# Kernel tuning notes

Hardware: AMD Instinct MI355X
Metric: run time of the kernel (lower is better)

Reference implementation:

```python
import jax, jax.numpy as jnp
import numpy as np

N_Q = 50000
B, T = 256, 500
DK = 128      # q_embed_dim == memory_key_state_dim == final_fc_dim
DV = 256      # qa_embed_dim == memory_value_state_dim
M = 50        # memory_size

def setup_inputs() -> dict:
    key = jax.random.key(0)
    ks = jax.random.split(key, 12)
    q_data = jax.random.randint(ks[0], (B, T), 0, N_Q + 1)
    qa_data = jax.random.randint(ks[1], (B, T), 0, 2 * N_Q + 1)
    # target in {-1, 0, 1}; -1 = padding (masked out)
    u = jax.random.uniform(ks[2], (B * T, 1))
    target = jnp.floor(u * 3.0) - 1.0
    # embedding tables with padding_idx=0 zeroed
    q_tab = (jax.random.normal(ks[3], (N_Q + 1, DK)) * (2.0 / DK) ** 0.5).at[0].set(0.0)
    qa_tab = (jax.random.normal(ks[4], (2 * N_Q + 1, DV)) * (2.0 / DV) ** 0.5).at[0].set(0.0)
    Mk = jax.random.normal(ks[5], (M, DK)) * (2.0 / DK) ** 0.5
    Mv0 = jax.random.normal(ks[6], (M, DV)) * (2.0 / DV) ** 0.5
    We = jax.random.normal(ks[7], (DV, DV)) * (1.0 / DV) ** 0.5
    be = jnp.zeros((DV,))
    Wa = jax.random.normal(ks[8], (DV, DV)) * (1.0 / DV) ** 0.5
    ba = jnp.zeros((DV,))
    Wr = jax.random.normal(ks[9], (DK, DV + DK)) * (2.0 / (DV + DK)) ** 0.5
    br = jnp.zeros((DK,))
    Wp = jax.random.normal(ks[10], (1, DK)) * (2.0 / DK) ** 0.5
    bp = jnp.zeros((1,))
    return dict(q_data=q_data, qa_data=qa_data, target=target, q_tab=q_tab,
                qa_tab=qa_tab, Mk=Mk, Mv0=Mv0, We=We, be=be, Wa=Wa, ba=ba,
                Wr=Wr, br=br, Wp=Wp, bp=bp)


def reference(q_data, qa_data, target, q_tab, qa_tab, Mk, Mv0, We, be, Wa, ba, Wr, br, Wp, bp):
    b, t = q_data.shape
    q_e = q_tab[q_data]            # (B,T,DK)
    qa_e = qa_tab[qa_data]         # (B,T,DV)
    wr_mask = (q_data >= 1).astype(q_e.dtype)  # write gate per step
    Mv_init = jnp.broadcast_to(Mv0[None], (b, M, DV))

    def step(Mv, xs):
        q, qa, m = xs              # q:(B,DK) qa:(B,DV) m:(B,)
        w = jax.nn.softmax(q @ Mk.T, axis=-1)          # (B,M) correlation weight
        read = jnp.einsum('bm,bmd->bd', w, Mv)         # (B,DV)
        e = jax.nn.sigmoid(qa @ We.T + be)             # erase (B,DV)
        a = jnp.tanh(qa @ Wa.T + ba)                   # add   (B,DV)
        new = Mv * (1.0 - w[:, :, None] * e[:, None, :]) + w[:, :, None] * a[:, None, :]
        Mv = jnp.where(m[:, None, None] > 0, new, Mv)  # only write for non-pad steps
        return Mv, read

    _, reads = jax.lax.scan(step, Mv_init,
                            (q_e.transpose(1, 0, 2), qa_e.transpose(1, 0, 2), wr_mask.T))
    reads = reads.transpose(1, 0, 2)                    # (B,T,DV)
    feat = jnp.concatenate([reads, q_e], axis=2).reshape(b * t, DV + DK)
    h = jnp.tanh(feat @ Wr.T + br)                      # (B*T,DK)
    pred = h @ Wp.T + bp                                # (B*T,1) logits
    mask = target >= 0
    # stable BCE-with-logits per element
    per = jnp.maximum(pred, 0.0) - pred * target + jnp.log1p(jnp.exp(-jnp.abs(pred)))
    n_valid = jnp.maximum(jnp.sum(mask.astype(pred.dtype)), 1.0)
    loss = jnp.sum(jnp.where(mask, per, 0.0)) / n_valid
    probs = jax.nn.sigmoid(pred)
    return loss, probs
```

## Files before the change

### kernel.cpp

```cpp
#include <hip/hip_runtime.h>
#include <hip/hip_bf16.h>
#include <stdint.h>


#define BATCH 256
#define TLEN  500
#define DKQ   128
#define DVV   256
#define MSZ   50
#define NROWS 128000
#define GSZ   10

__device__ __forceinline__ float bfs(uint16_t u){
  union { uint32_t u; float f; } v; v.u = ((uint32_t)u) << 16; return v.f;
}
__device__ __forceinline__ uint16_t f2b(float x){
  union { __hip_bfloat16 h; uint16_t u; } c; c.h = __float2bfloat16(x); return c.u;
}

typedef __attribute__((ext_vector_type(8))) short bf16x8;
typedef __attribute__((ext_vector_type(4))) float f32x4;

__device__ __forceinline__ void gl_lds16(const void* g, void* l){
  __builtin_amdgcn_global_load_lds(
      (const __attribute__((address_space(1))) void*)g,
      (__attribute__((address_space(3))) void*)l, 16, 0, 0);
}

__global__ __launch_bounds__(128, 1) void k_w(
    const int* __restrict__ q_data, const float* __restrict__ q_tab,
    const float* __restrict__ Mk, float* __restrict__ w_ws)
{
  __shared__ float mk[MSZ*DKQ];
  __shared__ float wt[128*52];
  const int tid = threadIdx.x;
  for (int li = tid; li < 1600; li += 128)
    ((float4*)mk)[li] = ((const float4*)Mk)[li];
  __syncthreads();

  const int row = blockIdx.x*128 + tid;
  const int qi = q_data[row];
  const float4* qrow = (const float4*)(q_tab + (size_t)qi*DKQ);

  float acc[MSZ];
  #pragma unroll
  for (int m=0;m<MSZ;m++) acc[m] = 0.f;

  #pragma unroll 1
  for (int c8=0; c8<8; c8++){
    float4 q0 = qrow[c8*4+0], q1 = qrow[c8*4+1], q2 = qrow[c8*4+2], q3 = qrow[c8*4+3];
    #pragma unroll
    for (int m=0;m<MSZ;m++){
      const float4* mr = (const float4*)&mk[m*DKQ + c8*16];
      float4 a = mr[0], b = mr[1], cc = mr[2], d = mr[3];
      float s = acc[m];
      s = fmaf(q0.x,a.x,s);  s = fmaf(q0.y,a.y,s);  s = fmaf(q0.z,a.z,s);  s = fmaf(q0.w,a.w,s);
      s = fmaf(q1.x,b.x,s);  s = fmaf(q1.y,b.y,s);  s = fmaf(q1.z,b.z,s);  s = fmaf(q1.w,b.w,s);
      s = fmaf(q2.x,cc.x,s); s = fmaf(q2.y,cc.y,s); s = fmaf(q2.z,cc.z,s); s = fmaf(q2.w,cc.w,s);
      s = fmaf(q3.x,d.x,s);  s = fmaf(q3.y,d.y,s);  s = fmaf(q3.z,d.z,s);  s = fmaf(q3.w,d.w,s);
      acc[m] = s;
    }
  }
  float mx = acc[0];
  #pragma unroll
  for (int m=1;m<MSZ;m++) mx = fmaxf(mx, acc[m]);
  float s = 0.f;
  #pragma unroll
  for (int m=0;m<MSZ;m++){ acc[m] = __expf(acc[m]-mx); s += acc[m]; }
  float inv = 1.0f / s;
  #pragma unroll
  for (int m=0;m<MSZ;m++) wt[tid*52+m] = acc[m]*inv;
  wt[tid*52+50] = 0.f; wt[tid*52+51] = 0.f;
  __syncthreads();
  float4* dst = (float4*)(w_ws + (size_t)blockIdx.x*128*52);
  const float4* src = (const float4*)wt;
  for (int li = tid; li < 1664; li += 128) dst[li] = src[li];
}

__global__ __launch_bounds__(256) void k_cvt(
    const float* __restrict__ qa_tab, const float* __restrict__ We,
    const float* __restrict__ Wa, uint16_t* __restrict__ qa_bf,
    uint16_t* __restrict__ wcomb)
{
  const size_t n_qa4 = 6400064;
  const size_t n_w4  = 32768;
  size_t stride = (size_t)gridDim.x*blockDim.x;
  for (size_t i = (size_t)blockIdx.x*256 + threadIdx.x; i < n_qa4 + n_w4; i += stride){
    float4 v;
    if (i < n_qa4){
      v = ((const float4*)qa_tab)[i];
      ushort4 o; o.x=f2b(v.x); o.y=f2b(v.y); o.z=f2b(v.z); o.w=f2b(v.w);
      ((ushort4*)qa_bf)[i] = o;
    } else {
      size_t j = i - n_qa4;
      size_t f = j*4;
      int col = (int)(f >> 8), k = (int)(f & 255);
      const float* srcp = (col < 256) ? (We + (size_t)col*256 + k)
                                      : (Wa + (size_t)(col-256)*256 + k);
      v = *(const float4*)srcp;
      ushort4 o; o.x=f2b(v.x); o.y=f2b(v.y); o.z=f2b(v.z); o.w=f2b(v.w);
      ((ushort4*)wcomb)[j] = o;
    }
  }
}

__global__ __launch_bounds__(256) void k_cvt2(
    const float* __restrict__ q_tab, const float* __restrict__ Wr,
    uint16_t* __restrict__ q_bf, uint16_t* __restrict__ wr_bf)
{
  const size_t n_q4  = 1600032;
  const size_t n_wr4 = 12288;
  size_t stride = (size_t)gridDim.x*blockDim.x;
  for (size_t i = (size_t)blockIdx.x*256 + threadIdx.x; i < n_q4 + n_wr4; i += stride){
    if (i < n_q4){
      float4 v = ((const float4*)q_tab)[i];
      ushort4 o; o.x=f2b(v.x); o.y=f2b(v.y); o.z=f2b(v.z); o.w=f2b(v.w);
      ((ushort4*)q_bf)[i] = o;
    } else {
      size_t j = i - n_q4;
      float4 v = ((const float4*)Wr)[j];
      ushort4 o; o.x=f2b(v.x); o.y=f2b(v.y); o.z=f2b(v.z); o.w=f2b(v.w);
      ((ushort4*)wr_bf)[j] = o;
    }
  }
}

__global__ __launch_bounds__(256, 2) void k_ea(
    const int* __restrict__ qa_data, const uint16_t* __restrict__ qa_bf,
    const uint16_t* __restrict__ wcomb, const float* __restrict__ be,
    const float* __restrict__ ba, __hip_bfloat16* __restrict__ ea_ws)
{
  __shared__ uint16_t Ab[128*32];
  __shared__ uint16_t Bb[128*32];
  const int tid = threadIdx.x;
  const int lane = tid & 63, wid = tid >> 6;
  const int braw = blockIdx.x;
  const int nb = (braw >> 3) & 3;
  const int mb = (braw & 7) | ((braw >> 5) << 3);
  const int rb = mb*128, cb = nb*128;

  const char* qac = (const char*)qa_bf;
  size_t aoff0, aoff1;
  {
    int r0 = wid*32 + (lane>>2);
    aoff0 = (size_t)qa_data[rb + r0]*512      + (size_t)(lane&3)*16;
    aoff1 = (size_t)qa_data[rb + r0 + 16]*512 + (size_t)(lane&3)*16;
  }
  const char* wcb = (const char*)wcomb;
  size_t boff0 = (size_t)(cb + wid*32 + (lane>>2))*512 + (size_t)(lane&3)*16;
  size_t boff1 = boff0 + 16*512;

  const int wr = (wid>>1)*64, wc = (wid&1)*64;
  float bias[4];
  #pragma unroll
  for (int tj=0;tj<4;tj++){
    int colg = cb + wc + tj*16 + (lane&15);
    bias[tj] = (nb<2) ? be[colg] : ba[colg-256];
  }

  f32x4 acc[4][4];
  #pragma unroll
  for (int i=0;i<4;i++){
    #pragma unroll
    for (int j=0;j<4;j++) acc[i][j] = (f32x4)(0.f);
  }

  #pragma unroll 1
  for (int kc=0; kc<8; kc++){
    __syncthreads();
    gl_lds16(qac + aoff0 + (size_t)kc*64, &Ab[(wid*2+0)*512]);
    gl_lds16(qac + aoff1 + (size_t)kc*64, &Ab[(wid*2+1)*512]);
    gl_lds16(wcb + boff0 + (size_t)kc*64, &Bb[(wid*2+0)*512]);
    gl_lds16(wcb + boff1 + (size_t)kc*64, &Bb[(wid*2+1)*512]);
    __syncthreads();
    bf16x8 af[4], bfr[4];
    #pragma unroll
    for (int ti=0;ti<4;ti++)
      af[ti] = *(const bf16x8*)&Ab[(wr + ti*16 + (lane&15))*32 + (lane>>4)*8];
    #pragma unroll
    for (int tj=0;tj<4;tj++)
      bfr[tj] = *(const bf16x8*)&Bb[(wc + tj*16 + (lane&15))*32 + (lane>>4)*8];
    #pragma unroll
    for (int ti=0;ti<4;ti++){
      #pragma unroll
      for (int tj=0;tj<4;tj++)
        acc[ti][tj] = __builtin_amdgcn_mfma_f32_16x16x32_bf16(af[ti], bfr[tj], acc[ti][tj], 0, 0, 0);
    }
  }
  const int rq = (lane>>4)*4, cl = lane&15;
  #pragma unroll
  for (int ti=0;ti<4;ti++){
    #pragma unroll
    for (int r=0;r<4;r++){
      int row = rb + wr + ti*16 + rq + r;
      __hip_bfloat16* orow = ea_ws + (size_t)row*512 + cb + wc;
      #pragma unroll
      for (int tj=0;tj<4;tj++){
        float x = acc[ti][tj][r] + bias[tj];
        float v = (nb<2) ? (1.f/(1.f+__expf(-x)))
                         : (1.f - 2.f/(__expf(2.f*x)+1.f));
        orow[tj*16 + cl] = __float2bfloat16(v);
      }
    }
  }
}

__global__ __launch_bounds__(256, 1) void k_scan(
    const int* __restrict__ q_data, const float* __restrict__ w_ws,
    const uint16_t* __restrict__ ea_ws, const float* __restrict__ Mv0,
    __hip_bfloat16* __restrict__ reads_ws)
{
  __shared__ __align__(16) float wlds[2][GSZ*52];
  const int tid  = threadIdx.x;
  const int d    = tid;
  const int b    = blockIdx.x;
  const int base = b * TLEN;

  float Mv[52];
  #pragma unroll
  for (int m=0;m<MSZ;m++) Mv[m] = Mv0[(size_t)m*256 + d];
  Mv[50] = 0.f; Mv[51] = 0.f;

  typedef const __attribute__((address_space(4))) int cint;
  cint* qbase = (cint*)q_data + base;

  const char* wsrc = (const char*)(w_ws + (size_t)base*52);
  if (tid < 130)
    gl_lds16(wsrc + (size_t)tid*16, &wlds[0][(tid>>6)*256]);

  uint32_t epk[GSZ], epn[GSZ];
  #pragma unroll
  for (int j=0;j<GSZ;j++){
    uint32_t e16 = ea_ws[(size_t)(base+j)*512 + d];
    uint32_t a16 = ea_ws[(size_t)(base+j)*512 + 256 + d];
    epk[j] = (a16 << 16) | e16;
  }
  asm volatile("s_waitcnt vmcnt(0)");
  __syncthreads();

  #pragma unroll 1
  for (int g=0; g<50; g++){
    if (g < 49){
      if (tid < 130)
        gl_lds16(wsrc + (size_t)(g+1)*2080 + (size_t)tid*16,
                 &wlds[(g+1)&1][(tid>>6)*256]);
      const int sn = base + (g+1)*GSZ;
      #pragma unroll
      for (int j=0;j<GSZ;j++){
        uint32_t e16 = ea_ws[(size_t)(sn+j)*512 + d];
        uint32_t a16 = ea_ws[(size_t)(sn+j)*512 + 256 + d];
        epn[j] = (a16 << 16) | e16;
      }
    }
    int qv[GSZ];
    #pragma unroll
    for (int j=0;j<GSZ;j++) qv[j] = qbase[g*GSZ + j];

    const float* wb = wlds[g&1];
    #pragma unroll
    for (int jj=0; jj<GSZ; jj++){
      const f32x4* wq = (const f32x4*)(wb + jj*52);
      const uint32_t p = epk[jj];
      union { uint32_t u; float f; } ue_, ua_;
      ue_.u = p << 16; ua_.u = p & 0xffff0000u;
      const float ef = ue_.f, af = ua_.f;

      f32x4 wv[13];
      #pragma unroll
      for (int qq=0;qq<13;qq++) wv[qq] = wq[qq];

      float r0=0.f, r1=0.f, r2=0.f, r3=0.f;
      #pragma unroll
      for (int qq=0;qq<13;qq++){
        r0 = fmaf(wv[qq].x, Mv[qq*4+0], r0);
        r1 = fmaf(wv[qq].y, Mv[qq*4+1], r1);
        r2 = fmaf(wv[qq].z, Mv[qq*4+2], r2);
        r3 = fmaf(wv[qq].w, Mv[qq*4+3], r3);
      }
      reads_ws[(size_t)(base + g*GSZ + jj)*256 + d] =
          __float2bfloat16((r0+r1)+(r2+r3));

      if (qv[jj] > 0){
        #pragma unroll
        for (int qq=0;qq<13;qq++){
          { float tt = fmaf(ef, Mv[qq*4+0], -af); Mv[qq*4+0] = fmaf(-wv[qq].x, tt, Mv[qq*4+0]); }
          { float tt = fmaf(ef, Mv[qq*4+1], -af); Mv[qq*4+1] = fmaf(-wv[qq].y, tt, Mv[qq*4+1]); }
          { float tt = fmaf(ef, Mv[qq*4+2], -af); Mv[qq*4+2] = fmaf(-wv[qq].z, tt, Mv[qq*4+2]); }
          { float tt = fmaf(ef, Mv[qq*4+3], -af); Mv[qq*4+3] = fmaf(-wv[qq].w, tt, Mv[qq*4+3]); }
        }
      }
    }

    if (g < 49){
      #pragma unroll
      for (int j=0;j<GSZ;j++) epk[j] = epn[j];
    }
    asm volatile("s_waitcnt vmcnt(0)");
    __syncthreads();
  }
}

__global__ __launch_bounds__(256, 2) void k_final(
    const int* __restrict__ q_data, const uint16_t* __restrict__ q_bf,
    const uint16_t* __restrict__ reads16, const uint16_t* __restrict__ wr_bf,
    const float* __restrict__ br, const float* __restrict__ Wp,
    const float* __restrict__ bp, const float* __restrict__ target,
    float* __restrict__ out, float* __restrict__ parts)
{
  __shared__ uint16_t Ab[64*32];
  __shared__ uint16_t Bb[128*32];
  __shared__ float redbuf[8];
  const int tid = threadIdx.x;
  const int lane = tid & 63, wid = tid >> 6;
  const int rb = blockIdx.x * 64;

  const char* rdc = (const char*)reads16;
  const char* qbc = (const char*)q_bf;
  const char* wrc = (const char*)wr_bf;
  const int arow = wid*16 + (lane>>2);
  size_t aoff_r = (size_t)(rb+arow)*512 + (size_t)(lane&3)*16;
  size_t aoff_q = (size_t)q_data[rb+arow]*256 + (size_t)(lane&3)*16;
  size_t boff0  = (size_t)(wid*32 + (lane>>2))*768 + (size_t)(lane&3)*16;
  size_t boff1  = boff0 + 16*768;

  f32x4 acc[8];
  #pragma unroll
  for (int tj=0;tj<8;tj++) acc[tj] = (f32x4)(0.f);

  #pragma unroll 1
  for (int kc=0; kc<12; kc++){
    __syncthreads();
    if (kc < 8) gl_lds16(rdc + aoff_r + (size_t)kc*64,     &Ab[wid*512]);
    else        gl_lds16(qbc + aoff_q + (size_t)(kc-8)*64, &Ab[wid*512]);
    gl_lds16(wrc + boff0 + (size_t)kc*64, &Bb[(wid*2+0)*512]);
    gl_lds16(wrc + boff1 + (size_t)kc*64, &Bb[(wid*2+1)*512]);
    __syncthreads();
    bf16x8 af = *(const bf16x8*)&Ab[(wid*16 + (lane&15))*32 + (lane>>4)*8];
    #pragma unroll
    for (int tj=0;tj<8;tj++){
      bf16x8 bf = *(const bf16x8*)&Bb[(tj*16 + (lane&15))*32 + (lane>>4)*8];
      acc[tj] = __builtin_amdgcn_mfma_f32_16x16x32_bf16(af, bf, acc[tj], 0, 0, 0);
    }
  }
  const int cl = lane & 15, rq = lane >> 4;
  float p[4] = {0.f,0.f,0.f,0.f};
  #pragma unroll
  for (int tj=0;tj<8;tj++){
    int cg = tj*16 + cl;
    float brv = br[cg], wpv = Wp[cg];
    #pragma unroll
    for (int r=0;r<4;r++){
      float x = acc[tj][r] + brv;
      float hh = 1.f - 2.f/(__expf(2.f*x)+1.f);
      p[r] = fmaf(hh, wpv, p[r]);
    }
  }
  #pragma unroll
  for (int off=1; off<16; off<<=1){
    #pragma unroll
    for (int r=0;r<4;r++) p[r] += __shfl_xor(p[r], off);
  }
  float bpv = bp[0];
  float lsum = 0.f, csum = 0.f;
  if (cl == 0){
    #pragma unroll
    for (int r=0;r<4;r++){
      int row = rb + wid*16 + rq*4 + r;
      float pred = p[r] + bpv;
      out[1 + row] = 1.f/(1.f + __expf(-pred));
      float tg = target[row];
      if (tg >= 0.f){
        lsum += fmaxf(pred, 0.f) - pred*tg + log1pf(__expf(-fabsf(pred)));
        csum += 1.f;
      }
    }
  }
  #pragma unroll
  for (int off=16; off<64; off<<=1){
    lsum += __shfl_xor(lsum, off);
    csum += __shfl_xor(csum, off);
  }
  if (lane == 0){ redbuf[wid*2] = lsum; redbuf[wid*2+1] = csum; }
  __syncthreads();
  if (tid == 0){
    parts[blockIdx.x]        = redbuf[0]+redbuf[2]+redbuf[4]+redbuf[6];
    parts[2000 + blockIdx.x] = redbuf[1]+redbuf[3]+redbuf[5]+redbuf[7];
  }
}

__global__ __launch_bounds__(256) void k_loss(
    const float* __restrict__ parts, float* __restrict__ out)
{
  __shared__ float red[8];
  const int tid = threadIdx.x;
  float l = 0.f, cn = 0.f;
  for (int i = tid; i < 2000; i += 256){ l += parts[i]; cn += parts[2000+i]; }
  #pragma unroll
  for (int off=32; off>0; off>>=1){ l += __shfl_xor(l, off); cn += __shfl_xor(cn, off); }
  if ((tid & 63) == 0){ red[(tid>>6)*2] = l; red[(tid>>6)*2+1] = cn; }
  __syncthreads();
  if (tid == 0){
    float L = red[0]+red[2]+red[4]+red[6];
    float C = red[1]+red[3]+red[5]+red[7];
    out[0] = L / fmaxf(C, 1.f);
  }
}

extern "C" void kernel_launch(void* const* d_in, const int* in_sizes, int n_in,
                              void* d_out, int out_size, void* d_ws, size_t ws_size,
                              hipStream_t stream) {
  const int*   q_data  = (const int*)d_in[0];
  const int*   qa_data = (const int*)d_in[1];
  const float* target  = (const float*)d_in[2];
  const float* q_tab   = (const float*)d_in[3];
  const float* qa_tab  = (const float*)d_in[4];
  const float* Mk  = (const float*)d_in[5];
  const float* Mv0 = (const float*)d_in[6];
  const float* We  = (const float*)d_in[7];
  const float* be  = (const float*)d_in[8];
  const float* Wa  = (const float*)d_in[9];
  const float* ba  = (const float*)d_in[10];
  const float* Wr  = (const float*)d_in[11];
  const float* br  = (const float*)d_in[12];
  const float* Wp  = (const float*)d_in[13];
  const float* bp  = (const float*)d_in[14];

  char* ws = (char*)d_ws;
  float*          w_ws     = (float*)ws;
  __hip_bfloat16* ea_ws    = (__hip_bfloat16*)(ws + 26624000);
  uint16_t*       qa_bf    = (uint16_t*)(ws + 157696000);
  uint16_t*       wcomb    = (uint16_t*)(ws + 208896512);
  __hip_bfloat16* reads_ws = (__hip_bfloat16*)(ws + 157696000);
  float*          parts    = (float*)ws;
  uint16_t*       q_bf     = (uint16_t*)(ws + 2000000);
  uint16_t*       wr_bf    = (uint16_t*)(ws + 16000000);

  float* out = (float*)d_out;

  k_w    <<<1000, 128, 0, stream>>>(q_data, q_tab, Mk, w_ws);
  k_cvt  <<<2048, 256, 0, stream>>>(qa_tab, We, Wa, qa_bf, wcomb);
  k_ea   <<<4000, 256, 0, stream>>>(qa_data, qa_bf, wcomb, be, ba, ea_ws);
  k_scan <<<256,  256, 0, stream>>>(q_data, w_ws, (const uint16_t*)ea_ws, Mv0, reads_ws);
  k_cvt2 <<<1024, 256, 0, stream>>>(q_tab, Wr, q_bf, wr_bf);
  k_final<<<2000, 256, 0, stream>>>(q_data, q_bf, (const uint16_t*)reads_ws, wr_bf, br, Wp, bp, target, out, parts);
  k_loss <<<1,    256, 0, stream>>>(parts, out);
}
```

Before: 701.7 us.

## Split scan memory slots across half-waves and double scan grid to 512 blocks

```diff
diff --git a/kernel.cpp b/kernel.cpp
--- a/kernel.cpp
+++ b/kernel.cpp
@@ -205,21 +205,27 @@
   }
 }
 
-__global__ __launch_bounds__(256, 1) void k_scan(
+__global__ __launch_bounds__(256, 2) void k_scan(
     const int* __restrict__ q_data, const float* __restrict__ w_ws,
     const uint16_t* __restrict__ ea_ws, const float* __restrict__ Mv0,
     __hip_bfloat16* __restrict__ reads_ws)
 {
-  __shared__ __align__(16) float wlds[2][GSZ*52];
+  __shared__ __align__(16) float wlds[2][GSZ*52 + 4];
   const int tid  = threadIdx.x;
-  const int d    = tid;
-  const int b    = blockIdx.x;
+  const int lane = tid & 63;
+  const int wid  = tid >> 6;
+  const int h    = lane >> 5;
+  const int b    = blockIdx.x & 255;
+  const int dblk = blockIdx.x >> 8;
+  const int d    = dblk*128 + wid*32 + (lane & 31);
   const int base = b * TLEN;
 
-  float Mv[52];
-  #pragma unroll
-  for (int m=0;m<MSZ;m++) Mv[m] = Mv0[(size_t)m*256 + d];
-  Mv[50] = 0.f; Mv[51] = 0.f;
+  float Mv[28];
+  #pragma unroll
+  for (int i=0;i<28;i++){
+    int m = h*28 + i;
+    Mv[i] = (m < MSZ) ? Mv0[(size_t)m*256 + d] : 0.f;
+  }
 
   typedef const __attribute__((address_space(4))) int cint;
   cint* qbase = (cint*)q_data + base;
@@ -256,38 +262,41 @@
     #pragma unroll
     for (int j=0;j<GSZ;j++) qv[j] = qbase[g*GSZ + j];
 
-    const float* wb = wlds[g&1];
+    const float* wbuf = wlds[g&1];
     #pragma unroll
     for (int jj=0; jj<GSZ; jj++){
-      const f32x4* wq = (const f32x4*)(wb + jj*52);
+      const f32x4* wq = (const f32x4*)(wbuf + jj*52 + h*28);
+      f32x4 w0=wq[0], w1=wq[1], w2=wq[2], w3=wq[3], w4=wq[4], w5=wq[5], w6=wq[6];
+      if (h) w6 = (f32x4)(0.f);
+
       const uint32_t p = epk[jj];
       union { uint32_t u; float f; } ue_, ua_;
       ue_.u = p << 16; ua_.u = p & 0xffff0000u;
       const float ef = ue_.f, af = ua_.f;
 
-      f32x4 wv[13];
-      #pragma unroll
-      for (int qq=0;qq<13;qq++) wv[qq] = wq[qq];
-
       float r0=0.f, r1=0.f, r2=0.f, r3=0.f;
-      #pragma unroll
-      for (int qq=0;qq<13;qq++){
-        r0 = fmaf(wv[qq].x, Mv[qq*4+0], r0);
-        r1 = fmaf(wv[qq].y, Mv[qq*4+1], r1);
-        r2 = fmaf(wv[qq].z, Mv[qq*4+2], r2);
-        r3 = fmaf(wv[qq].w, Mv[qq*4+3], r3);
-      }
-      reads_ws[(size_t)(base + g*GSZ + jj)*256 + d] =
-          __float2bfloat16((r0+r1)+(r2+r3));
+      r0=fmaf(w0.x,Mv[0],r0);  r1=fmaf(w0.y,Mv[1],r1);  r2=fmaf(w0.z,Mv[2],r2);  r3=fmaf(w0.w,Mv[3],r3);
+      r0=fmaf(w1.x,Mv[4],r0);  r1=fmaf(w1.y,Mv[5],r1);  r2=fmaf(w1.z,Mv[6],r2);  r3=fmaf(w1.w,Mv[7],r3);
+      r0=fmaf(w2.x,Mv[8],r0);  r1=fmaf(w2.y,Mv[9],r1);  r2=fmaf(w2.z,Mv[10],r2); r3=fmaf(w2.w,Mv[11],r3);
+      r0=fmaf(w3.x,Mv[12],r0); r1=fmaf(w3.y,Mv[13],r1); r2=fmaf(w3.z,Mv[14],r2); r3=fmaf(w3.w,Mv[15],r3);
+      r0=fmaf(w4.x,Mv[16],r0); r1=fmaf(w4.y,Mv[17],r1); r2=fmaf(w4.z,Mv[18],r2); r3=fmaf(w4.w,Mv[19],r3);
+      r0=fmaf(w5.x,Mv[20],r0); r1=fmaf(w5.y,Mv[21],r1); r2=fmaf(w5.z,Mv[22],r2); r3=fmaf(w5.w,Mv[23],r3);
+      r0=fmaf(w6.x,Mv[24],r0); r1=fmaf(w6.y,Mv[25],r1); r2=fmaf(w6.z,Mv[26],r2); r3=fmaf(w6.w,Mv[27],r3);
+      float rp = (r0+r1)+(r2+r3);
+      float rs = rp + __shfl_xor(rp, 32);
+      if (h == 0)
+        reads_ws[(size_t)(base + g*GSZ + jj)*256 + d] = __float2bfloat16(rs);
 
       if (qv[jj] > 0){
-        #pragma unroll
-        for (int qq=0;qq<13;qq++){
-          { float tt = fmaf(ef, Mv[qq*4+0], -af); Mv[qq*4+0] = fmaf(-wv[qq].x, tt, Mv[qq*4+0]); }
-          { float tt = fmaf(ef, Mv[qq*4+1], -af); Mv[qq*4+1] = fmaf(-wv[qq].y, tt, Mv[qq*4+1]); }
-          { float tt = fmaf(ef, Mv[qq*4+2], -af); Mv[qq*4+2] = fmaf(-wv[qq].z, tt, Mv[qq*4+2]); }
-          { float tt = fmaf(ef, Mv[qq*4+3], -af); Mv[qq*4+3] = fmaf(-wv[qq].w, tt, Mv[qq*4+3]); }
-        }
+        #define UPD(W, I) { float tt = fmaf(ef, Mv[I], -af); Mv[I] = fmaf(-(W), tt, Mv[I]); }
+        UPD(w0.x,0)  UPD(w0.y,1)  UPD(w0.z,2)  UPD(w0.w,3)
+        UPD(w1.x,4)  UPD(w1.y,5)  UPD(w1.z,6)  UPD(w1.w,7)
+        UPD(w2.x,8)  UPD(w2.y,9)  UPD(w2.z,10) UPD(w2.w,11)
+        UPD(w3.x,12) UPD(w3.y,13) UPD(w3.z,14) UPD(w3.w,15)
+        UPD(w4.x,16) UPD(w4.y,17) UPD(w4.z,18) UPD(w4.w,19)
+        UPD(w5.x,20) UPD(w5.y,21) UPD(w5.z,22) UPD(w5.w,23)
+        UPD(w6.x,24) UPD(w6.y,25) UPD(w6.z,26) UPD(w6.w,27)
+        #undef UPD
       }
     }
 
@@ -440,7 +449,7 @@
   k_w    <<<1000, 128, 0, stream>>>(q_data, q_tab, Mk, w_ws);
   k_cvt  <<<2048, 256, 0, stream>>>(qa_tab, We, Wa, qa_bf, wcomb);
   k_ea   <<<4000, 256, 0, stream>>>(qa_data, qa_bf, wcomb, be, ba, ea_ws);
-  k_scan <<<256,  256, 0, stream>>>(q_data, w_ws, (const uint16_t*)ea_ws, Mv0, reads_ws);
+  k_scan <<<512,  256, 0, stream>>>(q_data, w_ws, (const uint16_t*)ea_ws, Mv0, reads_ws);
   k_cvt2 <<<1024, 256, 0, stream>>>(q_tab, Wr, q_bf, wr_bf);
   k_final<<<2000, 256, 0, stream>>>(q_data, q_bf, (const uint16_t*)reads_ws, wr_bf, br, Wp, bp, target, out, parts);
   k_loss <<<1,    256, 0, stream>>>(parts, out);
```

After: 613.1 us. -12.6%, faster.
